# Kernel tuning notes

Hardware: AMD Instinct MI355X
Metric: run time of the kernel (lower is better)

The kernel has to match this reference:

```python
import jax, jax.numpy as jnp
import numpy as np

DEGREE_RES = 15
NUM_ROT = int(np.ceil(360 / DEGREE_RES))  # 24
PIXEL_SIZE = 0.0625
IM_METERS = 4.0
IM_SIZE = int(IM_METERS / PIXEL_SIZE)  # 64


def _create_rot_mat():
    angles = np.radians([i * DEGREE_RES for i in range(NUM_ROT)])
    c, s = np.cos(angles), np.sin(angles)
    rot = np.stack([
        np.stack([c, np.zeros_like(c), -s], axis=-1),
        np.stack([np.zeros_like(c), np.ones_like(c), np.zeros_like(c)], axis=-1),
        np.stack([s, np.zeros_like(c), c], axis=-1),
    ], axis=1)  # [NUM_ROT, 3, 3]
    return jnp.asarray(rot, dtype=jnp.float32)


def setup_inputs() -> dict:
    key = jax.random.key(0)
    xyz = jax.random.normal(key, (32, 16384, 3), dtype=jnp.float32)
    rot_mat = _create_rot_mat()
    return {"xyz": xyz, "rot_mat": rot_mat}


def reference(xyz, rot_mat):
    B, N, _ = xyz.shape
    R = rot_mat.shape[0]
    # rotate each point by each rotation: [B, R, N, 3]
    xyz_rot = jnp.einsum('rij,bnj->brni', rot_mat, xyz)
    # project x,z -> pixel indices (offset by half image extent, 2 meters)
    proj = jnp.round((xyz_rot[..., :2] + IM_METERS / 2) / PIXEL_SIZE).astype(jnp.int32)
    mask = ((proj[..., 0] >= 0) & (proj[..., 0] < IM_SIZE) &
            (proj[..., 1] >= 0) & (proj[..., 1] < IM_SIZE))
    # out-of-range points are zeroed -> they (faithfully) write at pixel (0,0)
    proj = proj * mask[..., None]
    vals = xyz_rot[..., 2] / 10.0  # non-occupancy branch: scatter z/10
    image = jnp.zeros((B, R, IM_SIZE, IM_SIZE), dtype=xyz.dtype)
    b = jnp.arange(B)[:, None, None]
    r = jnp.arange(R)[None, :, None]
    image = image.at[b, r, proj[..., 1], proj[..., 0]].set(vals)
    return image
```

## Files before the change

### kernel.cpp

```cpp
#include <hip/hip_runtime.h>
#include <stdint.h>

#define BB 32
#define NN 16384
#define RR 24
#define IMS 64
#define NPIX (IMS * IMS)
#define RPB 3
#define GROUPS (RR / RPB)
#define SCRATCH (RPB * 64)
#define LDSN (RPB * NPIX + SCRATCH)

__global__ __launch_bounds__(1024) void rotproj_lds(
    const float* __restrict__ xyz, const float* __restrict__ rot,
    float* __restrict__ out) {
  __shared__ unsigned int img[LDSN];

  const int blk = blockIdx.x;
  const int b = blk >> 3;
  const int rg = blk & (GROUPS - 1);

  for (int i = threadIdx.x; i < LDSN; i += 1024) img[i] = 0u;

  const float* m = rot + rg * RPB * 9;
  float c0[RPB], c2[RPB], c6[RPB], c8[RPB];
#pragma unroll
  for (int rl = 0; rl < RPB; ++rl) {
    c0[rl] = m[rl * 9 + 0];
    c2[rl] = m[rl * 9 + 2];
    c6[rl] = m[rl * 9 + 6];
    c8[rl] = m[rl * 9 + 8];
  }

  const int lane = threadIdx.x & 63;
  int soff[RPB];
#pragma unroll
  for (int rl = 0; rl < RPB; ++rl) soff[rl] = RPB * NPIX + rl * 64 + lane;

  __syncthreads();

  const float4* base4 = (const float4*)(xyz + (size_t)b * NN * 3);

#pragma unroll
  for (int iter = 0; iter < 2; ++iter) {
    const int n0 = iter * 8192 + threadIdx.x * 8;
    const int v = 6 * (n0 >> 3);
    const float4 f0 = base4[v + 0];
    const float4 f1 = base4[v + 1];
    const float4 f2 = base4[v + 2];
    const float4 f3 = base4[v + 3];
    const float4 f4 = base4[v + 4];
    const float4 f5 = base4[v + 5];

    const float xs[8] = {f0.x, f0.w, f1.z, f2.y, f3.x, f3.w, f4.z, f5.y};
    const float ys[8] = {f0.y, f1.x, f1.w, f2.z, f3.y, f4.x, f4.w, f5.z};
    const float zs[8] = {f0.z, f1.y, f2.x, f2.w, f3.z, f4.y, f5.x, f5.w};

#pragma unroll
    for (int j = 0; j < 8; ++j) {
      const float x = xs[j], y = ys[j], z = zs[j];

      const int py = (int)rintf(__fmaf_rn(y, 16.0f, 32.0f));
      const bool pyin = (unsigned)py < (unsigned)IMS;
      const int pybase = py * IMS;
      const unsigned int nkey = (unsigned)(n0 + j + 1) << 17;

#pragma unroll
      for (int rl = 0; rl < RPB; ++rl) {
        const float xr =
            __fadd_rn(__fmul_rn(c0[rl], x), __fmul_rn(c2[rl], z));
        const float zr = __fmaf_rn(c6[rl], x, __fmul_rn(c8[rl], z));

        const int px = (int)rintf(__fmaf_rn(xr, 16.0f, 32.0f));
        const bool in = ((unsigned)px < (unsigned)IMS) & pyin;

        const unsigned int key = nkey | (__float_as_uint(zr) >> 15);

        const int inaddr = rl * NPIX + pybase + (px ^ py);
        const int a = in ? inaddr : soff[rl];
        atomicMax(&img[a], key);
      }
    }
  }

  __syncthreads();

  if (threadIdx.x < SCRATCH) {
    const unsigned int k = img[RPB * NPIX + threadIdx.x];
    if (k) atomicMax(&img[(threadIdx.x >> 6) * NPIX], k);
  }

  __syncthreads();

  float* oslice = out + ((size_t)b * RR + (size_t)rg * RPB) * NPIX;
#pragma unroll
  for (int t = 0; t < RPB * NPIX / 1024; ++t) {
    const int i = t * 1024 + threadIdx.x;
    const int py = (i >> 6) & (IMS - 1);
    const unsigned int k = img[(i & ~(IMS - 1)) | ((i & (IMS - 1)) ^ py)];
    const float zr = __uint_as_float((k & 0x1FFFFu) << 15);
    oslice[i] = k ? (zr / 10.0f) : 0.0f;
  }
}

extern "C" void kernel_launch(void* const* d_in, const int* in_sizes, int n_in,
                              void* d_out, int out_size, void* d_ws,
                              size_t ws_size, hipStream_t stream) {
  const float* xyz = (const float*)d_in[0];
  const float* rot = (const float*)d_in[1];
  float* out = (float*)d_out;

  rotproj_lds<<<BB * GROUPS, 1024, 0, stream>>>(xyz, rot, out);
}
```

Baseline: 71.21 us.

## Use wave-strided point loads and additive LDS swizzle for scatter atomics

Points are now loaded so consecutive lanes handle consecutive points (stride-64 per unrolled step) instead of each thread taking 8 contiguous points through float4 loads. The LDS pixel swizzle changes from XOR with py to an additive rotation by 37*py mod 64, applied both in the scatter and in the readback, and the scratch offset is folded into the per-rotation base. The aim is to cut LDS bank conflicts on the atomicMax scatter, since neighbouring lanes now hold neighbouring points. In exchange the global loads become scalar 12-byte-strided accesses rather than wide float4 loads.

```diff
diff --git a/kernel.cpp b/kernel.cpp
--- a/kernel.cpp
+++ b/kernel.cpp
@@ -32,38 +32,39 @@
     c8[rl] = m[rl * 9 + 8];
   }
 
+  const int w = threadIdx.x >> 6;
   const int lane = threadIdx.x & 63;
-  int soff[RPB];
+  int srel[RPB];
 #pragma unroll
-  for (int rl = 0; rl < RPB; ++rl) soff[rl] = RPB * NPIX + rl * 64 + lane;
+  for (int rl = 0; rl < RPB; ++rl)
+    srel[rl] = (RPB - rl) * NPIX + rl * 64 + lane;
 
   __syncthreads();
 
-  const float4* base4 = (const float4*)(xyz + (size_t)b * NN * 3);
+  const float* pts = xyz + (size_t)b * NN * 3;
 
 #pragma unroll
   for (int iter = 0; iter < 2; ++iter) {
-    const int n0 = iter * 8192 + threadIdx.x * 8;
-    const int v = 6 * (n0 >> 3);
-    const float4 f0 = base4[v + 0];
-    const float4 f1 = base4[v + 1];
-    const float4 f2 = base4[v + 2];
-    const float4 f3 = base4[v + 3];
-    const float4 f4 = base4[v + 4];
-    const float4 f5 = base4[v + 5];
-
-    const float xs[8] = {f0.x, f0.w, f1.z, f2.y, f3.x, f3.w, f4.z, f5.y};
-    const float ys[8] = {f0.y, f1.x, f1.w, f2.z, f3.y, f4.x, f4.w, f5.z};
-    const float zs[8] = {f0.z, f1.y, f2.x, f2.w, f3.z, f4.y, f5.x, f5.w};
+    const int nbase = w * 1024 + iter * 512 + lane;
+    float X[8], Y[8], Z[8];
+#pragma unroll
+    for (int jj = 0; jj < 8; ++jj) {
+      const float* p = pts + 3 * (nbase + jj * 64);
+      X[jj] = p[0];
+      Y[jj] = p[1];
+      Z[jj] = p[2];
+    }
 
 #pragma unroll
-    for (int j = 0; j < 8; ++j) {
-      const float x = xs[j], y = ys[j], z = zs[j];
+    for (int jj = 0; jj < 8; ++jj) {
+      const float x = X[jj], y = Y[jj], z = Z[jj];
+      const int n = nbase + jj * 64;
 
       const int py = (int)rintf(__fmaf_rn(y, 16.0f, 32.0f));
       const bool pyin = (unsigned)py < (unsigned)IMS;
       const int pybase = py * IMS;
-      const unsigned int nkey = (unsigned)(n0 + j + 1) << 17;
+      const int s = 37 * py;
+      const unsigned int nkey = (unsigned)(n + 1) << 17;
 
 #pragma unroll
       for (int rl = 0; rl < RPB; ++rl) {
@@ -76,9 +77,9 @@
 
         const unsigned int key = nkey | (__float_as_uint(zr) >> 15);
 
-        const int inaddr = rl * NPIX + pybase + (px ^ py);
-        const int a = in ? inaddr : soff[rl];
-        atomicMax(&img[a], key);
+        const int slot = pybase + ((px + s) & 63);
+        const int word = in ? slot : srel[rl];
+        atomicMax(&img[rl * NPIX + word], key);
       }
     }
   }
@@ -97,7 +98,8 @@
   for (int t = 0; t < RPB * NPIX / 1024; ++t) {
     const int i = t * 1024 + threadIdx.x;
     const int py = (i >> 6) & (IMS - 1);
-    const unsigned int k = img[(i & ~(IMS - 1)) | ((i & (IMS - 1)) ^ py)];
+    const int px = i & (IMS - 1);
+    const unsigned int k = img[(i & ~(IMS - 1)) | ((px + 37 * py) & 63)];
     const float zr = __uint_as_float((k & 0x1FFFFu) << 15);
     oslice[i] = k ? (zr / 10.0f) : 0.0f;
   }
```

After: 71.50 us. Within noise of the previous version (+0.4%).
